# Kernel optimization log

Hardware: AMD Instinct MI355X
Metric: run time of the kernel (lower is better)

Reference implementation:

```python
import jax, jax.numpy as jnp
import numpy as np
import math

H = 1024   # d_model
N = 64     # state size; N//2 complex modes
L_LEN = 4096


def setup_inputs() -> dict:
    key = jax.random.key(0)
    k1, k2 = jax.random.split(key)
    # S4D init: log_dt uniform in [log(dt_min), log(dt_max)]
    log_dt = jax.random.uniform(k1, (H,), dtype=jnp.float32) * (
        math.log(0.1) - math.log(0.001)) + math.log(0.001)
    # C complex, stored as real view (channels=1, H, N/2, 2)
    C_real = jax.random.normal(k2, (1, H, N // 2, 2), dtype=jnp.float32)
    log_A_real = jnp.log(0.5 * jnp.ones((H, N // 2), dtype=jnp.float32))
    A_imag = math.pi * jnp.tile(jnp.arange(N // 2, dtype=jnp.float32), (H, 1))
    return {"log_dt": log_dt, "C_real": C_real, "log_A_real": log_A_real,
            "A_imag": A_imag, "L": L_LEN}


def reference(log_dt, C_real, log_A_real, A_imag, L):
    # materialize_parms
    dt = jnp.exp(log_dt)                                  # (H,)
    A = -jnp.exp(log_A_real) + 1j * A_imag                # (H, N/2) complex
    C = C_real[..., 0] + 1j * C_real[..., 1]              # (1, H, N/2) complex
    # discretize (bilinear)
    dtA = A * dt[:, None]                                 # (H, N/2)
    B = dt[:, None] / (1.0 - dtA / 2)                     # (H, N/2)
    dC = C * B                                            # (1, H, N/2)
    dA = (1.0 + dtA / 2) / (1.0 - dtA / 2)                # (H, N/2)
    # log-Vandermonde: K[c,h,l] = 2*Re sum_n dC[c,h,n] * dA[h,n]**l
    x = jnp.log(dA)                                       # (H, N/2) complex
    ls = jnp.arange(L)                                    # (L,)
    V = jnp.exp(x[..., None] * ls)                        # (H, N/2, L) complex
    K = 2.0 * jnp.real(jnp.einsum('chn,hnl->chl', dC, V)) # (1, H, L)
    return K
```

## Files before the change

kernel.cpp:

```cpp
#include <hip/hip_runtime.h>
#include <hip/hip_bf16.h>
#include <math.h>

#define MODES 32
#define BLOCK 256
#define TWO_PI 6.283185307179586f
#define INV_2PI 0.15915494309189535f
#define LROWW 36

typedef __attribute__((ext_vector_type(8))) short bf16x8;
typedef __attribute__((ext_vector_type(4))) float f32x4;

__device__ __forceinline__ unsigned int pk_bf16(float a, float b) {
    __hip_bfloat162 h = __float22bfloat162_rn(float2{a, b});
    union { __hip_bfloat162 v; unsigned int u; } cv; cv.v = h;
    return cv.u;
}

__device__ __forceinline__ void split2(float a, float b, unsigned int& hi, unsigned int& lo) {
    hi = pk_bf16(a, b);
    const float ha = __uint_as_float((hi & 0xFFFFu) << 16);
    const float hb = __uint_as_float(hi & 0xFFFF0000u);
    lo = pk_bf16(a - ha, b - hb);
}

__global__ __launch_bounds__(BLOCK) void s4d_mfma(
    const float* __restrict__ log_dt,
    const float* __restrict__ C_real,
    const float* __restrict__ log_A_real,
    const float* __restrict__ A_imag,
    float* __restrict__ out)
{
    __shared__ __align__(16) unsigned int sAhi[64 * LROWW];
    __shared__ __align__(16) unsigned int sAlo[64 * LROWW];
    __shared__ __align__(16) unsigned int sBhi[64 * LROWW];
    __shared__ __align__(16) unsigned int sBlo[64 * LROWW];

    const int h = blockIdx.x;
    const int t = threadIdx.x;
    const int mode = t & 31;
    const int i8   = t >> 5;

    const float dt = __expf(log_dt[h]);
    const float ar = -__expf(log_A_real[h * MODES + mode]);
    const float ai = A_imag[h * MODES + mode];
    const float dtAr = ar * dt, dtAi = ai * dt;
    const float den_r = 1.0f - 0.5f * dtAr, den_i = -0.5f * dtAi;
    const float num_r = 1.0f + 0.5f * dtAr, num_i =  0.5f * dtAi;
    const float inv = 1.0f / (den_r * den_r + den_i * den_i);
    const float Br =  dt * den_r * inv;
    const float Bi = -dt * den_i * inv;
    const float Cr = C_real[(h * MODES + mode) * 2 + 0];
    const float Ci = C_real[(h * MODES + mode) * 2 + 1];
    const float dcr2 = 2.0f * (Cr * Br - Ci * Bi);
    const float dci2 = 2.0f * (Cr * Bi + Ci * Br);
    const float dAr = (num_r * den_r + num_i * den_i) * inv;
    const float dAi = (num_i * den_r - num_r * den_i) * inv;
    const float xr  = 0.5f * __logf(dAr * dAr + dAi * dAi);
    const float rev = atan2f(dAi, dAr) * INV_2PI;

    const float mag64 = __expf(64.0f * xr);
    float r64 = 64.0f * rev; r64 -= rintf(r64);
    float w_s, w_c; __sincosf(r64 * TWO_PI, &w_s, &w_c);
    const float Wr = mag64 * w_c, Wi = mag64 * w_s;

    const float s = (float)(i8 * 8);
    float er = __expf(xr * s);
    float ph = rev * s; ph -= rintf(ph);
    float sn, cs; __sincosf(ph * TWO_PI, &sn, &cs);
    float br = er * cs, bi = er * sn;
    float mags = __expf(64.0f * xr * s);
    float ph2 = r64 * s; ph2 -= rintf(ph2);
    float sn2, cs2; __sincosf(ph2 * TWO_PI, &sn2, &cs2);
    const float wsr = mags * cs2, wsi = mags * sn2;
    float pr = dcr2 * wsr - dci2 * wsi;
    float pi = dcr2 * wsi + dci2 * wsr;

    int base = (i8 * 8) * LROWW + mode;
    #pragma unroll
    for (int b = 0; b < 8; ++b) {
        unsigned int hi, lo;
        split2(br, bi, hi, lo);
        sBhi[base] = hi; sBlo[base] = lo;
        split2(pr, -pi, hi, lo);
        sAhi[base] = hi; sAlo[base] = lo;
        const float nbr = fmaf(br, dAr, -(bi * dAi));
        const float nbi = fmaf(br, dAi,   bi * dAr);
        br = nbr; bi = nbi;
        const float npr = fmaf(pr, Wr, -(pi * Wi));
        const float npi = fmaf(pr, Wi,   pi * Wr);
        pr = npr; pi = npi;
        base += LROWW;
    }
    __syncthreads();

    const int wv   = t >> 6;
    const int lane = t & 63;
    const int c16  = lane & 15;
    const int quad = lane >> 4;

    const int arow = (wv * 16 + c16) * LROWW + quad * 4;
    const bf16x8 ah0 = *(const bf16x8*)&sAhi[arow];
    const bf16x8 ah1 = *(const bf16x8*)&sAhi[arow + 16];
    const bf16x8 al0 = *(const bf16x8*)&sAlo[arow];
    const bf16x8 al1 = *(const bf16x8*)&sAlo[arow + 16];

    float* op = out + ((size_t)h << 12) + (size_t)(wv * 16 + quad * 4) * 64 + c16;

    #pragma unroll
    for (int nt = 0; nt < 4; ++nt) {
        const int brow = (nt * 16 + c16) * LROWW + quad * 4;
        const bf16x8 bh0 = *(const bf16x8*)&sBhi[brow];
        const bf16x8 bh1 = *(const bf16x8*)&sBhi[brow + 16];
        const bf16x8 bl0 = *(const bf16x8*)&sBlo[brow];
        const bf16x8 bl1 = *(const bf16x8*)&sBlo[brow + 16];

        f32x4 acc = {0.f, 0.f, 0.f, 0.f};
        acc = __builtin_amdgcn_mfma_f32_16x16x32_bf16(ah0, bh0, acc, 0, 0, 0);
        acc = __builtin_amdgcn_mfma_f32_16x16x32_bf16(ah1, bh1, acc, 0, 0, 0);
        acc = __builtin_amdgcn_mfma_f32_16x16x32_bf16(ah0, bl0, acc, 0, 0, 0);
        acc = __builtin_amdgcn_mfma_f32_16x16x32_bf16(ah1, bl1, acc, 0, 0, 0);
        acc = __builtin_amdgcn_mfma_f32_16x16x32_bf16(al0, bh0, acc, 0, 0, 0);
        acc = __builtin_amdgcn_mfma_f32_16x16x32_bf16(al1, bh1, acc, 0, 0, 0);

        #pragma unroll
        for (int r = 0; r < 4; ++r)
            op[(size_t)r * 64 + nt * 16] = acc[r];
    }
}

__global__ __launch_bounds__(BLOCK) void s4d_recur(
    const float* __restrict__ log_dt, const float* __restrict__ C_real,
    const float* __restrict__ log_A_real, const float* __restrict__ A_imag,
    float* __restrict__ out, int L)
{
    const int h = blockIdx.x, tid = threadIdx.x;
    const int P = L / BLOCK;
    __shared__ float4 s_c0[MODES], s_c1[MODES];
    if (tid < MODES) {
        const int n = tid;
        const float dt = __expf(log_dt[h]);
        const float ar = -__expf(log_A_real[h * MODES + n]);
        const float ai = A_imag[h * MODES + n];
        const float dtAr = ar * dt, dtAi = ai * dt;
        const float den_r = 1.0f - 0.5f * dtAr, den_i = -0.5f * dtAi;
        const float num_r = 1.0f + 0.5f * dtAr, num_i = 0.5f * dtAi;
        const float inv = 1.0f / (den_r * den_r + den_i * den_i);
        const float Brr = dt * den_r * inv, Bii = -dt * den_i * inv;
        const float Cr = C_real[(h * MODES + n) * 2 + 0];
        const float Ci = C_real[(h * MODES + n) * 2 + 1];
        const float dCr = Cr * Brr - Ci * Bii, dCi = Cr * Bii + Ci * Brr;
        const float dAr = (num_r * den_r + num_i * den_i) * inv;
        const float dAi = (num_i * den_r - num_r * den_i) * inv;
        const float xr = 0.5f * __logf(dAr * dAr + dAi * dAi);
        const float rev = atan2f(dAi, dAr) * INV_2PI;
        const float S = (float)BLOCK;
        const float mag = __expf(xr * S);
        float tt = rev * S; tt -= rintf(tt);
        float ws, wc; __sincosf(tt * TWO_PI, &ws, &wc);
        s_c0[n] = make_float4(xr, rev, 2.0f * dCr, 2.0f * dCi);
        s_c1[n] = make_float4(mag * wc, mag * ws, 2.0f * mag * wc, -(mag * mag));
    }
    __syncthreads();
    float m0[MODES], m1[MODES], aS[MODES], bS[MODES];
    float acc0 = 0.f, acc1 = 0.f;
    const float lf = (float)tid;
    #pragma unroll
    for (int n = 0; n < MODES; ++n) {
        const float4 c0 = s_c0[n]; const float4 c1 = s_c1[n];
        const float er = __expf(c0.x * lf);
        float tt = c0.y * lf; tt -= rintf(tt);
        float sn, cs; __sincosf(tt * TWO_PI, &sn, &cs);
        const float pr = er * cs, pi = er * sn;
        const float v0 = fmaf(c0.z, pr, -c0.w * pi);
        const float qr = fmaf(pr, c1.x, -pi * c1.y);
        const float qi = fmaf(pr, c1.y, pi * c1.x);
        const float v1 = fmaf(c0.z, qr, -c0.w * qi);
        m0[n] = v0; m1[n] = v1; acc0 += v0; acc1 += v1;
        aS[n] = c1.z; bS[n] = c1.w;
    }
    float* outp = out + (size_t)h * (size_t)L + tid;
    outp[0] = acc0;
    if (P > 1) outp[BLOCK] = acc1;
    int p = 2;
    for (; p + 1 < P; p += 2) {
        float accA = 0.f, accB = 0.f;
        #pragma unroll
        for (int n = 0; n < MODES; ++n) {
            const float mA = fmaf(aS[n], m1[n], bS[n] * m0[n]);
            const float mB = fmaf(aS[n], mA, bS[n] * m1[n]);
            accA += mA; accB += mB; m0[n] = mA; m1[n] = mB;
        }
        outp[(size_t)p * BLOCK] = accA;
        outp[(size_t)(p + 1) * BLOCK] = accB;
    }
    if (p < P) {
        float accA = 0.f;
        #pragma unroll
        for (int n = 0; n < MODES; ++n) {
            const float mA = fmaf(aS[n], m1[n], bS[n] * m0[n]);
            accA += mA; m0[n] = m1[n]; m1[n] = mA;
        }
        outp[(size_t)p * BLOCK] = accA;
    }
}

extern "C" void kernel_launch(void* const* d_in, const int* in_sizes, int n_in,
                              void* d_out, int out_size, void* d_ws, size_t ws_size,
                              hipStream_t stream) {
    const float* log_dt     = (const float*)d_in[0];
    const float* C_real     = (const float*)d_in[1];
    const float* log_A_real = (const float*)d_in[2];
    const float* A_imag     = (const float*)d_in[3];
    float* out = (float*)d_out;

    const int H = in_sizes[0];
    const int L = out_size / H;

    if (L == 4096) {
        s4d_mfma<<<H, BLOCK, 0, stream>>>(log_dt, C_real, log_A_real, A_imag, out);
    } else {
        s4d_recur<<<H, BLOCK, 0, stream>>>(log_dt, C_real, log_A_real, A_imag, out, L);
    }
}
```

Measured before the change: 69.88 us.

## Split each channel across two blocks and share per-mode constants via LDS

The grid is doubled so each channel is handled by two blocks, each computing half of the 64 output columns of the 64x64 output tile. Per-mode discretization constants are computed once by 32 threads and broadcast through shared memory, removing the redundant log/atan2/exp work from all 256 threads. The B operand tile is halved, and the launch bounds request 5 blocks per CU. The trade-off is that the A-side powers are recomputed in both blocks and an extra barrier is added.

```diff
diff --git a/kernel.cpp b/kernel.cpp
--- a/kernel.cpp
+++ b/kernel.cpp
@@ -24,7 +24,7 @@
     lo = pk_bf16(a - ha, b - hb);
 }
 
-__global__ __launch_bounds__(BLOCK) void s4d_mfma(
+__global__ __launch_bounds__(BLOCK, 5) void s4d_mfma(
     const float* __restrict__ log_dt,
     const float* __restrict__ C_real,
     const float* __restrict__ log_A_real,
@@ -33,64 +33,91 @@
 {
     __shared__ __align__(16) unsigned int sAhi[64 * LROWW];
     __shared__ __align__(16) unsigned int sAlo[64 * LROWW];
-    __shared__ __align__(16) unsigned int sBhi[64 * LROWW];
-    __shared__ __align__(16) unsigned int sBlo[64 * LROWW];
-
-    const int h = blockIdx.x;
-    const int t = threadIdx.x;
+    __shared__ __align__(16) unsigned int sBhi[32 * LROWW];
+    __shared__ __align__(16) unsigned int sBlo[32 * LROWW];
+    __shared__ __align__(16) float s_cst[MODES][8];
+
+    const int h  = blockIdx.x >> 1;
+    const int jh = blockIdx.x & 1;
+    const int t  = threadIdx.x;
     const int mode = t & 31;
-    const int i8   = t >> 5;
-
-    const float dt = __expf(log_dt[h]);
-    const float ar = -__expf(log_A_real[h * MODES + mode]);
-    const float ai = A_imag[h * MODES + mode];
-    const float dtAr = ar * dt, dtAi = ai * dt;
-    const float den_r = 1.0f - 0.5f * dtAr, den_i = -0.5f * dtAi;
-    const float num_r = 1.0f + 0.5f * dtAr, num_i =  0.5f * dtAi;
-    const float inv = 1.0f / (den_r * den_r + den_i * den_i);
-    const float Br =  dt * den_r * inv;
-    const float Bi = -dt * den_i * inv;
-    const float Cr = C_real[(h * MODES + mode) * 2 + 0];
-    const float Ci = C_real[(h * MODES + mode) * 2 + 1];
-    const float dcr2 = 2.0f * (Cr * Br - Ci * Bi);
-    const float dci2 = 2.0f * (Cr * Bi + Ci * Br);
-    const float dAr = (num_r * den_r + num_i * den_i) * inv;
-    const float dAi = (num_i * den_r - num_r * den_i) * inv;
-    const float xr  = 0.5f * __logf(dAr * dAr + dAi * dAi);
-    const float rev = atan2f(dAi, dAr) * INV_2PI;
-
-    const float mag64 = __expf(64.0f * xr);
+    const int g    = t >> 5;
+
+    if (t < MODES) {
+        const int n = t;
+        const float dt = __expf(log_dt[h]);
+        const float ar = -__expf(log_A_real[h * MODES + n]);
+        const float ai = A_imag[h * MODES + n];
+        const float dtAr = ar * dt, dtAi = ai * dt;
+        const float den_r = 1.0f - 0.5f * dtAr, den_i = -0.5f * dtAi;
+        const float num_r = 1.0f + 0.5f * dtAr, num_i =  0.5f * dtAi;
+        const float inv = 1.0f / (den_r * den_r + den_i * den_i);
+        const float Br =  dt * den_r * inv;
+        const float Bi = -dt * den_i * inv;
+        const float Cr = C_real[(h * MODES + n) * 2 + 0];
+        const float Ci = C_real[(h * MODES + n) * 2 + 1];
+        const float dAr = (num_r * den_r + num_i * den_i) * inv;
+        const float dAi = (num_i * den_r - num_r * den_i) * inv;
+        const float xr  = 0.5f * __logf(dAr * dAr + dAi * dAi);
+        const float rev = atan2f(dAi, dAr) * INV_2PI;
+        const float mag64 = __expf(64.0f * xr);
+        float r64 = 64.0f * rev; r64 -= rintf(r64);
+        float w_s, w_c; __sincosf(r64 * TWO_PI, &w_s, &w_c);
+        s_cst[n][0] = xr;
+        s_cst[n][1] = rev;
+        s_cst[n][2] = 2.0f * (Cr * Br - Ci * Bi);
+        s_cst[n][3] = 2.0f * (Cr * Bi + Ci * Br);
+        s_cst[n][4] = dAr;
+        s_cst[n][5] = dAi;
+        s_cst[n][6] = mag64 * w_c;
+        s_cst[n][7] = mag64 * w_s;
+    }
+    __syncthreads();
+
+    const float4 c0 = *(const float4*)&s_cst[mode][0];
+    const float4 c1 = *(const float4*)&s_cst[mode][4];
+    const float xr = c0.x, rev = c0.y, dcr2 = c0.z, dci2 = c0.w;
+    const float dAr = c1.x, dAi = c1.y, Wr = c1.z, Wi = c1.w;
+    const float xr64 = 64.0f * xr;
     float r64 = 64.0f * rev; r64 -= rintf(r64);
-    float w_s, w_c; __sincosf(r64 * TWO_PI, &w_s, &w_c);
-    const float Wr = mag64 * w_c, Wi = mag64 * w_s;
-
-    const float s = (float)(i8 * 8);
-    float er = __expf(xr * s);
-    float ph = rev * s; ph -= rintf(ph);
-    float sn, cs; __sincosf(ph * TWO_PI, &sn, &cs);
-    float br = er * cs, bi = er * sn;
-    float mags = __expf(64.0f * xr * s);
-    float ph2 = r64 * s; ph2 -= rintf(ph2);
-    float sn2, cs2; __sincosf(ph2 * TWO_PI, &sn2, &cs2);
-    const float wsr = mags * cs2, wsi = mags * sn2;
-    float pr = dcr2 * wsr - dci2 * wsi;
-    float pi = dcr2 * wsi + dci2 * wsr;
-
-    int base = (i8 * 8) * LROWW + mode;
-    #pragma unroll
-    for (int b = 0; b < 8; ++b) {
-        unsigned int hi, lo;
-        split2(br, bi, hi, lo);
-        sBhi[base] = hi; sBlo[base] = lo;
-        split2(pr, -pi, hi, lo);
-        sAhi[base] = hi; sAlo[base] = lo;
-        const float nbr = fmaf(br, dAr, -(bi * dAi));
-        const float nbi = fmaf(br, dAi,   bi * dAr);
-        br = nbr; bi = nbi;
-        const float npr = fmaf(pr, Wr, -(pi * Wi));
-        const float npi = fmaf(pr, Wi,   pi * Wr);
-        pr = npr; pi = npi;
-        base += LROWW;
+
+    {
+        const float s = (float)(g * 8);
+        float mags = __expf(xr64 * s);
+        float ph2 = r64 * s; ph2 -= rintf(ph2);
+        float sn2, cs2; __sincosf(ph2 * TWO_PI, &sn2, &cs2);
+        const float wsr = mags * cs2, wsi = mags * sn2;
+        float pr = dcr2 * wsr - dci2 * wsi;
+        float pi = dcr2 * wsi + dci2 * wsr;
+        int base = (g * 8) * LROWW + mode;
+        #pragma unroll
+        for (int b = 0; b < 8; ++b) {
+            unsigned int hi, lo;
+            split2(pr, -pi, hi, lo);
+            sAhi[base] = hi; sAlo[base] = lo;
+            const float npr = fmaf(pr, Wr, -(pi * Wi));
+            const float npi = fmaf(pr, Wi,   pi * Wr);
+            pr = npr; pi = npi;
+            base += LROWW;
+        }
+    }
+    {
+        const float j0 = (float)(jh * 32 + g * 4);
+        float er = __expf(xr * j0);
+        float ph = rev * j0; ph -= rintf(ph);
+        float sn, cs; __sincosf(ph * TWO_PI, &sn, &cs);
+        float br = er * cs, bi = er * sn;
+        int base = (g * 4) * LROWW + mode;
+        #pragma unroll
+        for (int b = 0; b < 4; ++b) {
+            unsigned int hi, lo;
+            split2(br, bi, hi, lo);
+            sBhi[base] = hi; sBlo[base] = lo;
+            const float nbr = fmaf(br, dAr, -(bi * dAi));
+            const float nbi = fmaf(br, dAi,   bi * dAr);
+            br = nbr; bi = nbi;
+            base += LROWW;
+        }
     }
     __syncthreads();
 
@@ -105,10 +132,11 @@
     const bf16x8 al0 = *(const bf16x8*)&sAlo[arow];
     const bf16x8 al1 = *(const bf16x8*)&sAlo[arow + 16];
 
-    float* op = out + ((size_t)h << 12) + (size_t)(wv * 16 + quad * 4) * 64 + c16;
+    float* op = out + ((size_t)h << 12) + (size_t)(wv * 16 + quad * 4) * 64
+                    + jh * 32 + c16;
 
     #pragma unroll
-    for (int nt = 0; nt < 4; ++nt) {
+    for (int nt = 0; nt < 2; ++nt) {
         const int brow = (nt * 16 + c16) * LROWW + quad * 4;
         const bf16x8 bh0 = *(const bf16x8*)&sBhi[brow];
         const bf16x8 bh1 = *(const bf16x8*)&sBhi[brow + 16];
@@ -218,7 +246,7 @@
     const int L = out_size / H;
 
     if (L == 4096) {
-        s4d_mfma<<<H, BLOCK, 0, stream>>>(log_dt, C_real, log_A_real, A_imag, out);
+        s4d_mfma<<<H * 2, BLOCK, 0, stream>>>(log_dt, C_real, log_A_real, A_imag, out);
     } else {
         s4d_recur<<<H, BLOCK, 0, stream>>>(log_dt, C_real, log_A_real, A_imag, out, L);
     }
```

Result: no change. 70.68 us (+1.1%).

## Split each channel across four blocks and replace log/atan2 powers with repeated squaring

Applied to the files above, without the earlier changes.

Launches four blocks per channel, each computing 16 rows of the 64x64 output tile, so every wave issues one MFMA tile instead of four and the grid is four times larger. Powers of dA are now built by repeated complex squaring and binary-exponent selection instead of log/atan2/exp/sincos, and occupancy is hinted with launch_bounds(256,6). The cost is that each of the four blocks recomputes all 64 B rows, and repeated squaring to high powers may accumulate rounding error.

```diff
diff --git a/kernel.cpp b/kernel.cpp
--- a/kernel.cpp
+++ b/kernel.cpp
@@ -11,6 +11,11 @@
 typedef __attribute__((ext_vector_type(8))) short bf16x8;
 typedef __attribute__((ext_vector_type(4))) float f32x4;
 
+struct cf { float r, i; };
+__device__ __forceinline__ cf cmul(cf a, cf b) {
+    return cf{fmaf(a.r, b.r, -(a.i * b.i)), fmaf(a.r, b.i, a.i * b.r)};
+}
+
 __device__ __forceinline__ unsigned int pk_bf16(float a, float b) {
     __hip_bfloat162 h = __float22bfloat162_rn(float2{a, b});
     union { __hip_bfloat162 v; unsigned int u; } cv; cv.v = h;
@@ -24,22 +29,23 @@
     lo = pk_bf16(a - ha, b - hb);
 }
 
-__global__ __launch_bounds__(BLOCK) void s4d_mfma(
+__global__ __launch_bounds__(BLOCK, 6) void s4d_mfma(
     const float* __restrict__ log_dt,
     const float* __restrict__ C_real,
     const float* __restrict__ log_A_real,
     const float* __restrict__ A_imag,
     float* __restrict__ out)
 {
-    __shared__ __align__(16) unsigned int sAhi[64 * LROWW];
-    __shared__ __align__(16) unsigned int sAlo[64 * LROWW];
+    __shared__ __align__(16) unsigned int sAhi[16 * LROWW];
+    __shared__ __align__(16) unsigned int sAlo[16 * LROWW];
     __shared__ __align__(16) unsigned int sBhi[64 * LROWW];
     __shared__ __align__(16) unsigned int sBlo[64 * LROWW];
 
-    const int h = blockIdx.x;
-    const int t = threadIdx.x;
+    const int h  = blockIdx.x >> 2;
+    const int bq = blockIdx.x & 3;
+    const int t  = threadIdx.x;
     const int mode = t & 31;
-    const int i8   = t >> 5;
+    const int g    = t >> 5;
 
     const float dt = __expf(log_dt[h]);
     const float ar = -__expf(log_A_real[h * MODES + mode]);
@@ -52,45 +58,66 @@
     const float Bi = -dt * den_i * inv;
     const float Cr = C_real[(h * MODES + mode) * 2 + 0];
     const float Ci = C_real[(h * MODES + mode) * 2 + 1];
-    const float dcr2 = 2.0f * (Cr * Br - Ci * Bi);
-    const float dci2 = 2.0f * (Cr * Bi + Ci * Br);
-    const float dAr = (num_r * den_r + num_i * den_i) * inv;
-    const float dAi = (num_i * den_r - num_r * den_i) * inv;
-    const float xr  = 0.5f * __logf(dAr * dAr + dAi * dAi);
-    const float rev = atan2f(dAi, dAr) * INV_2PI;
-
-    const float mag64 = __expf(64.0f * xr);
-    float r64 = 64.0f * rev; r64 -= rintf(r64);
-    float w_s, w_c; __sincosf(r64 * TWO_PI, &w_s, &w_c);
-    const float Wr = mag64 * w_c, Wi = mag64 * w_s;
-
-    const float s = (float)(i8 * 8);
-    float er = __expf(xr * s);
-    float ph = rev * s; ph -= rintf(ph);
-    float sn, cs; __sincosf(ph * TWO_PI, &sn, &cs);
-    float br = er * cs, bi = er * sn;
-    float mags = __expf(64.0f * xr * s);
-    float ph2 = r64 * s; ph2 -= rintf(ph2);
-    float sn2, cs2; __sincosf(ph2 * TWO_PI, &sn2, &cs2);
-    const float wsr = mags * cs2, wsi = mags * sn2;
-    float pr = dcr2 * wsr - dci2 * wsi;
-    float pi = dcr2 * wsi + dci2 * wsr;
-
-    int base = (i8 * 8) * LROWW + mode;
-    #pragma unroll
-    for (int b = 0; b < 8; ++b) {
+    const cf dC2 = {2.0f * (Cr * Br - Ci * Bi), 2.0f * (Cr * Bi + Ci * Br)};
+    const cf dA  = {(num_r * den_r + num_i * den_i) * inv,
+                    (num_i * den_r - num_r * den_i) * inv};
+
+    cf p2 = cmul(dA, dA);
+    cf p4 = cmul(p2, p2);
+    cf p8 = cmul(p4, p4);
+    cf p16 = cmul(p8, p8);
+    cf p32 = cmul(p16, p16);
+    const cf W = cmul(p32, p32);
+    cf Wp[6];
+    Wp[0] = W;
+    Wp[1] = cmul(W, W);
+    Wp[2] = cmul(Wp[1], Wp[1]);
+    Wp[3] = cmul(Wp[2], Wp[2]);
+    Wp[4] = cmul(Wp[3], Wp[3]);
+    Wp[5] = cmul(Wp[4], Wp[4]);
+
+    {
+        const int i0 = 16 * bq + 2 * g;
+        cf wp = {1.0f, 0.0f};
+        #pragma unroll
+        for (int j = 0; j < 6; ++j) {
+            cf m = cmul(wp, Wp[j]);
+            const bool bit = (i0 >> j) & 1;
+            wp.r = bit ? m.r : wp.r;
+            wp.i = bit ? m.i : wp.i;
+        }
+        cf a0 = cmul(dC2, wp);
+        cf a1 = cmul(a0, W);
         unsigned int hi, lo;
-        split2(br, bi, hi, lo);
-        sBhi[base] = hi; sBlo[base] = lo;
-        split2(pr, -pi, hi, lo);
+        int base = (2 * g) * LROWW + mode;
+        split2(a0.r, -a0.i, hi, lo);
         sAhi[base] = hi; sAlo[base] = lo;
-        const float nbr = fmaf(br, dAr, -(bi * dAi));
-        const float nbi = fmaf(br, dAi,   bi * dAr);
-        br = nbr; bi = nbi;
-        const float npr = fmaf(pr, Wr, -(pi * Wi));
-        const float npi = fmaf(pr, Wi,   pi * Wr);
-        pr = npr; pi = npi;
-        base += LROWW;
+        split2(a1.r, -a1.i, hi, lo);
+        sAhi[base + LROWW] = hi; sAlo[base + LROWW] = lo;
+    }
+
+    {
+        cf E1 = p8;
+        cf E2 = cmul(E1, E1);
+        cf E4 = cmul(E2, E2);
+        cf b = {1.0f, 0.0f};
+        {
+            cf m = cmul(b, E1); bool bit = g & 1;
+            b.r = bit ? m.r : b.r; b.i = bit ? m.i : b.i;
+            m = cmul(b, E2); bit = (g >> 1) & 1;
+            b.r = bit ? m.r : b.r; b.i = bit ? m.i : b.i;
+            m = cmul(b, E4); bit = (g >> 2) & 1;
+            b.r = bit ? m.r : b.r; b.i = bit ? m.i : b.i;
+        }
+        int base = (8 * g) * LROWW + mode;
+        #pragma unroll
+        for (int k = 0; k < 8; ++k) {
+            unsigned int hi, lo;
+            split2(b.r, b.i, hi, lo);
+            sBhi[base] = hi; sBlo[base] = lo;
+            b = cmul(b, dA);
+            base += LROWW;
+        }
     }
     __syncthreads();
 
@@ -99,34 +126,31 @@
     const int c16  = lane & 15;
     const int quad = lane >> 4;
 
-    const int arow = (wv * 16 + c16) * LROWW + quad * 4;
+    const int arow = c16 * LROWW + quad * 4;
     const bf16x8 ah0 = *(const bf16x8*)&sAhi[arow];
     const bf16x8 ah1 = *(const bf16x8*)&sAhi[arow + 16];
     const bf16x8 al0 = *(const bf16x8*)&sAlo[arow];
     const bf16x8 al1 = *(const bf16x8*)&sAlo[arow + 16];
 
-    float* op = out + ((size_t)h << 12) + (size_t)(wv * 16 + quad * 4) * 64 + c16;
-
+    const int brow = (wv * 16 + c16) * LROWW + quad * 4;
+    const bf16x8 bh0 = *(const bf16x8*)&sBhi[brow];
+    const bf16x8 bh1 = *(const bf16x8*)&sBhi[brow + 16];
+    const bf16x8 bl0 = *(const bf16x8*)&sBlo[brow];
+    const bf16x8 bl1 = *(const bf16x8*)&sBlo[brow + 16];
+
+    f32x4 acc = {0.f, 0.f, 0.f, 0.f};
+    acc = __builtin_amdgcn_mfma_f32_16x16x32_bf16(ah0, bh0, acc, 0, 0, 0);
+    acc = __builtin_amdgcn_mfma_f32_16x16x32_bf16(ah1, bh1, acc, 0, 0, 0);
+    acc = __builtin_amdgcn_mfma_f32_16x16x32_bf16(ah0, bl0, acc, 0, 0, 0);
+    acc = __builtin_amdgcn_mfma_f32_16x16x32_bf16(ah1, bl1, acc, 0, 0, 0);
+    acc = __builtin_amdgcn_mfma_f32_16x16x32_bf16(al0, bh0, acc, 0, 0, 0);
+    acc = __builtin_amdgcn_mfma_f32_16x16x32_bf16(al1, bh1, acc, 0, 0, 0);
+
+    float* op = out + ((size_t)h << 12) + (size_t)(16 * bq + quad * 4) * 64
+                    + wv * 16 + c16;
     #pragma unroll
-    for (int nt = 0; nt < 4; ++nt) {
-        const int brow = (nt * 16 + c16) * LROWW + quad * 4;
-        const bf16x8 bh0 = *(const bf16x8*)&sBhi[brow];
-        const bf16x8 bh1 = *(const bf16x8*)&sBhi[brow + 16];
-        const bf16x8 bl0 = *(const bf16x8*)&sBlo[brow];
-        const bf16x8 bl1 = *(const bf16x8*)&sBlo[brow + 16];
-
-        f32x4 acc = {0.f, 0.f, 0.f, 0.f};
-        acc = __builtin_amdgcn_mfma_f32_16x16x32_bf16(ah0, bh0, acc, 0, 0, 0);
-        acc = __builtin_amdgcn_mfma_f32_16x16x32_bf16(ah1, bh1, acc, 0, 0, 0);
-        acc = __builtin_amdgcn_mfma_f32_16x16x32_bf16(ah0, bl0, acc, 0, 0, 0);
-        acc = __builtin_amdgcn_mfma_f32_16x16x32_bf16(ah1, bl1, acc, 0, 0, 0);
-        acc = __builtin_amdgcn_mfma_f32_16x16x32_bf16(al0, bh0, acc, 0, 0, 0);
-        acc = __builtin_amdgcn_mfma_f32_16x16x32_bf16(al1, bh1, acc, 0, 0, 0);
-
-        #pragma unroll
-        for (int r = 0; r < 4; ++r)
-            op[(size_t)r * 64 + nt * 16] = acc[r];
-    }
+    for (int r = 0; r < 4; ++r)
+        op[(size_t)r * 64] = acc[r];
 }
 
 __global__ __launch_bounds__(BLOCK) void s4d_recur(
@@ -218,7 +242,7 @@
     const int L = out_size / H;
 
     if (L == 4096) {
-        s4d_mfma<<<H, BLOCK, 0, stream>>>(log_dt, C_real, log_A_real, A_imag, out);
+        s4d_mfma<<<H * 4, BLOCK, 0, stream>>>(log_dt, C_real, log_A_real, A_imag, out);
     } else {
         s4d_recur<<<H, BLOCK, 0, stream>>>(log_dt, C_real, log_A_real, A_imag, out, L);
     }
```

Measured after the change: 73.42 us. 5.1% more time.
